# Kernel optimization log

Measured on AMD Instinct MI355X. Metric: run time of the kernel, lower is better.

The kernel has to match this reference:

```python
import jax, jax.numpy as jnp
import numpy as np

N_Q = 4; K = 4; IMG = 28; PAD = IMG + 2  # pad right/bottom so edge windows exist
N_WIN = 14 * 14  # stride-2 windows over 28x28


def _window_idx():
    # Faithful to torch: flatten the (possibly truncated) window row-major,
    # then pad with zeros AT THE END of the flattened vector.
    zero = PAD * PAD - 1  # padded image is zero there
    rows = []
    for i in range(0, IMG - 1, 2):
        for j in range(0, IMG - 1, 2):
            h = min(K, IMG - i); w = min(K, IMG - j)
            ids = [(i + r) * PAD + (j + c) for r in range(h) for c in range(w)]
            ids += [zero] * (K * K - len(ids))
            rows.append(ids)
    return np.asarray(rows, np.int32)  # [196, 16]

_WIDX = _window_idx()
# wire 0 is the most-significant bit of the 16-dim statevector index
_BITS = ((np.arange(16)[None, :] >> (3 - np.arange(4))[:, None]) & 1)
_ZSIGN = (1.0 - 2.0 * _BITS).astype(np.float32)  # [4, 16] PauliZ eigenvalues
# Four CRZ gates (control i, target (i+1)%4) are all diagonal -> combined diagonal phase
_CRZ_SIGNS = np.zeros(16, np.float32)
for _b in range(16):
    s = 0
    for _i in range(4):
        c = (_b >> (3 - _i)) & 1
        t = (_b >> (3 - ((_i + 1) % 4))) & 1
        s += c * (2 * t - 1)
    _CRZ_SIGNS[_b] = s
_H = (np.array([[1, 1], [1, -1]], np.complex64) / np.sqrt(2.0)).astype(np.complex64)


def _rz(a):  # a [B] -> [B,2,2]: diag(e^{-i a/2}, e^{+i a/2})
    em = jnp.exp(-0.5j * a); ep = jnp.exp(0.5j * a); z = jnp.zeros_like(em)
    return jnp.stack([jnp.stack([em, z], -1), jnp.stack([z, ep], -1)], -2)


def _ry(a):  # a [...] -> [...,2,2]
    c = jnp.cos(0.5 * a); s = jnp.sin(0.5 * a)
    return jnp.stack([jnp.stack([c, -s], -1), jnp.stack([s, c], -1)], -2).astype(jnp.complex64)


def _apply1q(state, U, w):  # state [B,16], U [B,2,2] or [2,2], wire w (0=MSB)
    L = 2 ** w; R = 2 ** (3 - w)
    s = state.reshape(-1, L, 2, R)
    if U.ndim == 2:
        out = jnp.einsum('ij,bajc->baic', U, s)
    else:
        out = jnp.einsum('bij,bajc->baic', U, s)
    return out.reshape(-1, 16)


def reference(x, crz_theta, ry_theta, fc1_w, fc1_b, fc2_w, fc2_b):
    B = x.shape[0]
    xp = jnp.pad(x[:, 0], ((0, 0), (0, 2), (0, 2))).reshape(B, -1)  # [B, 900]
    wins = xp[:, jnp.asarray(_WIDX)]              # [B, 196, 16]
    wins = jnp.transpose(wins, (1, 0, 2))         # [196, B, 16] for scan

    crz_diag = jnp.exp(0.5j * crz_theta * jnp.asarray(_CRZ_SIGNS))  # [16]
    Ry = _ry(ry_theta)                            # shared trainable RY, [2,2]
    H = jnp.asarray(_H)
    zsT = jnp.asarray(_ZSIGN).T                   # [16, 4]

    def step(state, f):  # state [B,16] complex64 persists ACROSS windows (no reset in source)
        for w in range(4):
            # compose H then the encoder rotations on this wire into one 2x2 per batch elem
            U = jnp.broadcast_to(H, (B, 2, 2))
            n = 5 if w < 3 else 1  # wire 3 only gets rz(f[15])
            for i in range(n):
                a = f[:, w * 5 + i]
                M = _rz(a) if i % 2 == 0 else _ry(a)  # gates = rz,ry,rz,ry,rz
                U = jnp.einsum('bij,bjk->bik', M, U)
            state = _apply1q(state, U, w)
        state = state * crz_diag[None, :]          # ring of CRZ gates (diagonal)
        for w in range(4):
            state = _apply1q(state, Ry, w)
        probs = state.real ** 2 + state.imag ** 2
        return state, probs @ zsT                  # [B, 4] PauliZ expectations

    state0 = jnp.zeros((B, 16), jnp.complex64).at[:, 0].set(1.0)
    _, outs = jax.lax.scan(step, state0, wins)     # [196, B, 4]
    feats = jnp.transpose(outs, (1, 0, 2)).reshape(B, N_WIN * 4)  # window-major concat
    h1 = feats @ fc1_w.T + fc1_b
    h1 = jnp.where(h1 > 0, h1, 0.1 * h1)           # LeakyReLU(0.1)
    return h1 @ fc2_w.T + fc2_b


def setup_inputs() -> dict:
    key = jax.random.key(0)
    ks = jax.random.split(key, 7)
    B = 16384
    return {
        'x': jax.random.normal(ks[0], (B, 1, 28, 28), jnp.float32),
        'crz_theta': jax.random.normal(ks[1], (), jnp.float32),
        'ry_theta': jax.random.normal(ks[2], (), jnp.float32),
        'fc1_w': jax.random.normal(ks[3], (20, 784), jnp.float32) * 0.03,
        'fc1_b': jnp.zeros((20,), jnp.float32),
        'fc2_w': jax.random.normal(ks[4], (2, 20), jnp.float32) * 0.1,
        'fc2_b': jnp.zeros((2,), jnp.float32),
    }
```

## Files before the change

### kernel.cpp

```cpp
#include <hip/hip_runtime.h>

#define RS2f 0.70710678118654752f

#define QP_XOR1 0xB1
#define QP_XOR2 0x4E
#define QP_BC0  0x00
#define QP_BC1  0x55
#define QP_BC2  0xAA
#define QP_BC3  0xFF

typedef float v2f __attribute__((ext_vector_type(2)));

template<int CTRL> __device__ __forceinline__ float dppf(float x) {
  return __int_as_float(__builtin_amdgcn_update_dpp(
      0, __float_as_int(x), CTRL, 0xF, 0xF, true));
}
template<int CTRL> __device__ __forceinline__ v2f dpp2(v2f v) {
  v2f r; r.x = dppf<CTRL>(v.x); r.y = dppf<CTRL>(v.y); return r;
}

__device__ __forceinline__ float sxor(float x, int sm) {
  return __int_as_float(__float_as_int(x) ^ sm);
}
__device__ __forceinline__ v2f vsplat(float a) { v2f r; r.x = a; r.y = a; return r; }
__device__ __forceinline__ v2f vperp(v2f v) { v2f r; r.x = -v.y; r.y = v.x; return r; }
__device__ __forceinline__ v2f vperc(v2f v) { v2f r; r.x = v.y; r.y = -v.x; return r; }
__device__ __forceinline__ v2f vfma2(float a, v2f b, v2f c) {
  return __builtin_elementwise_fma(vsplat(a), b, c);
}
__device__ __forceinline__ v2f vmul2(float a, v2f b) { return vsplat(a) * b; }

__device__ __forceinline__ void build_gate(float a0, float a1, float a2, float a3, float a4,
                                           float &w0r, float &w0i, float &w1r, float &w1i) {
  float sBp, cBp, sBm, cBm, sC, cC, sP, cP, sM, cM;
  __sincosf(0.5f * (a1 + a3), &sBp, &cBp);
  __sincosf(0.5f * (a1 - a3), &sBm, &cBm);
  __sincosf(0.5f * a2,        &sC,  &cC);
  __sincosf(0.5f * (a0 + a4), &sP,  &cP);
  __sincosf(0.5f * (a0 - a4), &sM,  &cM);
  float m00r =  cBp * cC, m00i = -cBm * sC;
  float m01r = -sBp * cC, m01i =  sBm * sC;
  float alr = fmaf(m00r, cP,  m00i * sP);
  float ali = fmaf(m00i, cP, -m00r * sP);
  float ber = fmaf(m01r, cM, -m01i * sM);
  float bei = fmaf(m01i, cM,  m01r * sM);
  w0r = RS2f * (alr + ber); w0i = RS2f * (ali + bei);
  w1r = RS2f * (alr - ber); w1i = RS2f * (ali - bei);
}

#define PICK_FULL                                                            \
  a0 = l0 ? P[0][0] : l1 ? P[1][1] : l2 ? P[2][2] : P[3][3];                 \
  a1 = l0 ? P[0][1] : l1 ? P[1][2] : l2 ? P[2][3] : 0.f;                     \
  a2 = l0 ? P[0][2] : l1 ? P[1][3] : l2 ? P[3][0] : 0.f;                     \
  a3 = l0 ? P[0][3] : l1 ? P[2][0] : l2 ? P[3][1] : 0.f;                     \
  a4 = l0 ? P[1][0] : l1 ? P[2][1] : l2 ? P[3][2] : 0.f;

#define PICK_W2                                                              \
  a0 = l0 ? P[0][0] : l1 ? P[2][1] : 0.f;                                    \
  a1 = l0 ? P[0][1] : l1 ? P[3][0] : 0.f;                                    \
  a2 = l0 ? P[1][0] : l1 ? P[3][1] : 0.f;                                    \
  a3 = l0 ? P[1][1] : 0.f;                                                   \
  a4 = l0 ? P[2][0] : 0.f;

#define PICK_H2                                                              \
  a0 = l0 ? P[0][0] : l1 ? P[1][1] : 0.f;                                    \
  a1 = l0 ? P[0][1] : l1 ? P[1][2] : 0.f;                                    \
  a2 = l0 ? P[0][2] : l1 ? P[1][3] : 0.f;                                    \
  a3 = l0 ? P[0][3] : 0.f;                                                   \
  a4 = l0 ? P[1][0] : 0.f;

#define PICK_22                                                              \
  a0 = l0 ? P[0][0] : 0.f;                                                   \
  a1 = l0 ? P[0][1] : 0.f;                                                   \
  a2 = l0 ? P[1][0] : 0.f;                                                   \
  a3 = l0 ? P[1][1] : 0.f;                                                   \
  a4 = 0.f;

#define APPLY_AND_FOLD(WIN) do {                                             \
                                \
  { float w0r = dppf<QP_BC0>(Wc0), w0i = dppf<QP_BC0>(Wc1);                  \
    float w1r = dppf<QP_BC0>(Wc2), w1i = dppf<QP_BC0>(Wc3);                  \
    float uar = sxor(w0r, sm0), uai = w0i;                                   \
    float ubr = w1r,            ubi = sxor(w1i, sm0);                        \
    _Pragma("unroll")                                                        \
    for (int k = 0; k < 4; ++k) {                                            \
      v2f p = dpp2<QP_XOR2>(s[k]);                                           \
      v2f a = s[k];                                                          \
      s[k] = vfma2(uar, a, vfma2(uai, vperp(a),                              \
                   vfma2(ubr, p, vmul2(ubi, vperp(p)))));                    \
    } }                                                                      \
                                 \
  { float w0r = dppf<QP_BC1>(Wc0), w0i = dppf<QP_BC1>(Wc1);                  \
    float w1r = dppf<QP_BC1>(Wc2), w1i = dppf<QP_BC1>(Wc3);                  \
    float uar = sxor(w0r, sm1), uai = w0i;                                   \
    float ubr = w1r,            ubi = sxor(w1i, sm1);                        \
    _Pragma("unroll")                                                        \
    for (int k = 0; k < 4; ++k) {                                            \
      v2f p = dpp2<QP_XOR1>(s[k]);                                           \
      v2f a = s[k];                                                          \
      s[k] = vfma2(uar, a, vfma2(uai, vperp(a),                              \
                   vfma2(ubr, p, vmul2(ubi, vperp(p)))));                    \
    } }                                                                      \
   \
  { float w0r = dppf<QP_BC2>(Wc0), w0i = dppf<QP_BC2>(Wc1);                  \
    float w1r = dppf<QP_BC2>(Wc2), w1i = dppf<QP_BC2>(Wc3);                  \
    float nw0r = -w0r, nw0i = -w0i;                                          \
    _Pragma("unroll")                                                        \
    for (int k = 0; k < 2; ++k) {                                            \
      v2f lo = s[k], hi = s[k+2];                                            \
      s[k]   = vfma2(w0r, lo, vfma2(w0i, vperp(lo),                          \
                     vfma2(w1r, hi, vmul2(w1i, vperp(hi)))));                \
      s[k+2] = vfma2(w1r, lo, vfma2(w1i, vperc(lo),                          \
                     vfma2(nw0r, hi, vmul2(nw0i, vperc(hi)))));              \
    } }                                                                      \
                                           \
  { float w0r = dppf<QP_BC3>(Wc0), w0i = dppf<QP_BC3>(Wc1);                  \
    float w1r = dppf<QP_BC3>(Wc2), w1i = dppf<QP_BC3>(Wc3);                  \
    float nw0r = -w0r, nw0i = -w0i;                                          \
    _Pragma("unroll")                                                        \
    for (int k = 0; k < 4; k += 2) {                                         \
      v2f lo = s[k], hi = s[k+1];                                            \
      s[k]   = vfma2(w0r, lo, vfma2(w0i, vperp(lo),                          \
                     vfma2(w1r, hi, vmul2(w1i, vperp(hi)))));                \
      s[k+1] = vfma2(w1r, lo, vfma2(w1i, vperc(lo),                          \
                     vfma2(nw0r, hi, vmul2(nw0i, vperc(hi)))));              \
    } }                                                                      \
                                    \
  _Pragma("unroll")                                                          \
  for (int k = 0; k < 4; ++k)                                                \
    s[k] = vfma2(czk[k], s[k], vmul2(szk[k], vperp(s[k])));                  \
                                              \
  _Pragma("unroll")                                                          \
  for (int k = 0; k < 4; ++k) {                                              \
    v2f p = dpp2<QP_XOR2>(s[k]);                                             \
    s[k] = vfma2(cry, s[k], vmul2(sgn0, p));                                 \
  }                                                                          \
  _Pragma("unroll")                                                          \
  for (int k = 0; k < 4; ++k) {                                              \
    v2f p = dpp2<QP_XOR1>(s[k]);                                             \
    s[k] = vfma2(cry, s[k], vmul2(sgn1, p));                                 \
  }                                                                          \
                                                   \
  _Pragma("unroll")                                                          \
  for (int k = 0; k < 2; ++k) {                                              \
    v2f lo = s[k], hi = s[k+2];                                              \
    s[k]   = vfma2(cry, lo, vmul2(nsry, hi));                                \
    s[k+2] = vfma2(sry, lo, vmul2(cry, hi));                                 \
  }                                                                          \
  _Pragma("unroll")                                                          \
  for (int k = 0; k < 4; k += 2) {                                           \
    v2f lo = s[k], hi = s[k+1];                                              \
    s[k]   = vfma2(cry, lo, vmul2(nsry, hi));                                \
    s[k+1] = vfma2(sry, lo, vmul2(cry, hi));                                 \
  }                                                                          \
                                        \
  { v2f q0 = s[0]*s[0], q1 = s[1]*s[1], q2 = s[2]*s[2], q3 = s[3]*s[3];      \
    float p0 = q0.x + q0.y, p1 = q1.x + q1.y;                                \
    float p2 = q2.x + q2.y, p3 = q3.x + q3.y;                                \
    float s01 = p0 + p1, s23 = p2 + p3;                                      \
    float t_  = s01 + s23;                                                   \
    float o0 = sxor(t_, sm0);                                                \
    float o1 = sxor(t_, sm1);                                                \
    float o2 = s01 - s23;                                                    \
    float o3 = (p0 - p1) + (p2 - p3);                                        \
    o0 += dppf<QP_XOR1>(o0); o0 += dppf<QP_XOR2>(o0);                        \
    o1 += dppf<QP_XOR1>(o1); o1 += dppf<QP_XOR2>(o1);                        \
    o2 += dppf<QP_XOR1>(o2); o2 += dppf<QP_XOR2>(o2);                        \
    o3 += dppf<QP_XOR1>(o3); o3 += dppf<QP_XOR2>(o3);                        \
    const int win4_ = (WIN) * 4;                                             \
    _Pragma("unroll")                                                        \
    for (int j = 0; j < 5; ++j) {                                            \
      float4 wv = *(const float4*)(swl + j * 784 + win4_);                   \
      h1[j] = fmaf(wv.x, o0, fmaf(wv.y, o1, fmaf(wv.z, o2, fmaf(wv.w, o3, h1[j])))); \
    } }                                                                      \
} while (0)

#define ROTATE_W  Wc0 = Wn0; Wc1 = Wn1; Wc2 = Wn2; Wc3 = Wn3;

__global__ void __launch_bounds__(256)
quanv_kernel(const float* __restrict__ x,
             const float* __restrict__ crz_t,
             const float* __restrict__ ry_t,
             const float* __restrict__ fc1_w,
             const float* __restrict__ fc1_b,
             const float* __restrict__ fc2_w,
             const float* __restrict__ fc2_b,
             float* __restrict__ out, int B)
{
  __shared__ float sw[20 * 784];
  const int tid = threadIdx.x;
  for (int i = tid; i < (20 * 784) / 4; i += 256)
    ((float4*)sw)[i] = ((const float4*)fc1_w)[i];
  __syncthreads();

  const int l = tid & 3;
  const int b = (blockIdx.x * 256 + tid) >> 2;
  if (b >= B) return;
  const float* img = x + (size_t)b * 784;
  const bool l0 = (l == 0), l1 = (l == 1), l2 = (l == 2);

  const float theta = crz_t[0];
  const float ryt   = ry_t[0];
  float cry, sry;
  __sincosf(0.5f * ryt, &sry, &cry);
  const float nsry = -sry;
  const float sgn0 = (l & 2) ? sry : -sry;
  const float sgn1 = (l & 1) ? sry : -sry;
  const int sm0 = (l & 2) ? (int)0x80000000 : 0;
  const int sm1 = (l & 1) ? (int)0x80000000 : 0;

  float g0,g1,g2,g3;
  if      (l == 0) { g0= 0.f; g1=-1.f; g2=-1.f; g3=0.f; }
  else if (l == 1) { g0=-1.f; g1=-2.f; g2= 0.f; g3=1.f; }
  else if (l == 2) { g0=-1.f; g1= 0.f; g2=-2.f; g3=1.f; }
  else             { g0= 0.f; g1= 1.f; g2= 1.f; g3=4.f; }
  float czk[4], szk[4];
  __sincosf(0.5f*theta*g0, &szk[0], &czk[0]);
  __sincosf(0.5f*theta*g1, &szk[1], &czk[1]);
  __sincosf(0.5f*theta*g2, &szk[2], &czk[2]);
  __sincosf(0.5f*theta*g3, &szk[3], &czk[3]);

  v2f s[4];
#pragma unroll
  for (int k = 0; k < 4; ++k) { s[k].x = 0.f; s[k].y = 0.f; }
  if (l == 0) s[0].x = 1.f;

  float h1[5];
#pragma unroll
  for (int j = 0; j < 5; ++j) h1[j] = 0.f;
  const float* swl = sw + 5 * l * 784;

  float P[4][4];
  float a0, a1, a2, a3, a4;
  float Wc0, Wc1, Wc2, Wc3, Wn0, Wn1, Wn2, Wn3;

#pragma unroll 1
  for (int wi = 0; wi < 13; ++wi) {
    const float* imgw = img + (2 * wi) * 28;

#pragma unroll
    for (int r = 0; r < 4; ++r) {
      float4 v = *(const float4*)(imgw + r * 28);
      P[r][0]=v.x; P[r][1]=v.y; P[r][2]=v.z; P[r][3]=v.w;
    }
    PICK_FULL;
    build_gate(a0, a1, a2, a3, a4, Wc0, Wc1, Wc2, Wc3);

#pragma unroll 1
    for (int wj = 1; wj <= 12; ++wj) {
      const int c0 = 2 * wj + 2;
#pragma unroll
      for (int r = 0; r < 4; ++r) {
        P[r][0] = P[r][2]; P[r][1] = P[r][3];
        float2 v = *(const float2*)(imgw + r * 28 + c0);
        P[r][2] = v.x; P[r][3] = v.y;
      }
      PICK_FULL;
      build_gate(a0, a1, a2, a3, a4, Wn0, Wn1, Wn2, Wn3);
      APPLY_AND_FOLD(wi * 14 + wj - 1);
      ROTATE_W;
    }

#pragma unroll
    for (int r = 0; r < 4; ++r) {
      P[r][0] = P[r][2]; P[r][1] = P[r][3]; P[r][2] = 0.f; P[r][3] = 0.f;
    }
    PICK_W2;
    build_gate(a0, a1, a2, a3, a4, Wn0, Wn1, Wn2, Wn3);
    APPLY_AND_FOLD(wi * 14 + 12);
    ROTATE_W;
    APPLY_AND_FOLD(wi * 14 + 13);
  }

  {
    const float* imgw = img + 26 * 28;
#pragma unroll
    for (int r = 0; r < 2; ++r) {
      float4 v = *(const float4*)(imgw + r * 28);
      P[r][0]=v.x; P[r][1]=v.y; P[r][2]=v.z; P[r][3]=v.w;
    }
#pragma unroll
    for (int r = 2; r < 4; ++r) { P[r][0]=0.f; P[r][1]=0.f; P[r][2]=0.f; P[r][3]=0.f; }
    PICK_H2;
    build_gate(a0, a1, a2, a3, a4, Wc0, Wc1, Wc2, Wc3);

#pragma unroll 1
    for (int wj = 1; wj <= 12; ++wj) {
      const int c0 = 2 * wj + 2;
      P[0][0]=P[0][2]; P[0][1]=P[0][3];
      P[1][0]=P[1][2]; P[1][1]=P[1][3];
      float2 v0 = *(const float2*)(imgw + c0);       P[0][2]=v0.x; P[0][3]=v0.y;
      float2 v1 = *(const float2*)(imgw + 28 + c0);  P[1][2]=v1.x; P[1][3]=v1.y;
      PICK_H2;
      build_gate(a0, a1, a2, a3, a4, Wn0, Wn1, Wn2, Wn3);
      APPLY_AND_FOLD(182 + wj - 1);
      ROTATE_W;
    }

    P[0][0]=P[0][2]; P[0][1]=P[0][3]; P[0][2]=0.f; P[0][3]=0.f;
    P[1][0]=P[1][2]; P[1][1]=P[1][3]; P[1][2]=0.f; P[1][3]=0.f;
    PICK_22;
    build_gate(a0, a1, a2, a3, a4, Wn0, Wn1, Wn2, Wn3);
    APPLY_AND_FOLD(182 + 12);
    ROTATE_W;
    APPLY_AND_FOLD(182 + 13);
  }

  float pa = 0.f, pb = 0.f;
#pragma unroll
  for (int j = 0; j < 5; ++j) {
    const int r = 5 * l + j;
    float v = h1[j] + fc1_b[r];
    v = (v > 0.f) ? v : 0.1f * v;
    pa = fmaf(fc2_w[r],      v, pa);
    pb = fmaf(fc2_w[20 + r], v, pb);
  }
  pa += dppf<QP_XOR1>(pa); pa += dppf<QP_XOR2>(pa);
  pb += dppf<QP_XOR1>(pb); pb += dppf<QP_XOR2>(pb);
  if (l == 0) {
    float2 res; res.x = pa + fc2_b[0]; res.y = pb + fc2_b[1];
    *(float2*)(out + (size_t)b * 2) = res;
  }
}

extern "C" void kernel_launch(void* const* d_in, const int* in_sizes, int n_in,
                              void* d_out, int out_size, void* d_ws, size_t ws_size,
                              hipStream_t stream) {
  const float* x      = (const float*)d_in[0];
  const float* crz_t  = (const float*)d_in[1];
  const float* ry_t   = (const float*)d_in[2];
  const float* fc1_w  = (const float*)d_in[3];
  const float* fc1_b  = (const float*)d_in[4];
  const float* fc2_w  = (const float*)d_in[5];
  const float* fc2_b  = (const float*)d_in[6];
  float* out = (float*)d_out;
  const int B = in_sizes[0] / 784;
  const int grid = (B * 4 + 255) / 256;
  quanv_kernel<<<grid, 256, 0, stream>>>(x, crz_t, ry_t, fc1_w, fc1_b,
                                         fc2_w, fc2_b, out, B);
}
```

Measured before the change: 225.0 us.

## Split each statevector across eight lanes instead of four

Each sample now runs on 8 lanes holding 2 amplitudes each instead of 4 lanes holding 4, so the grid doubles. The third qubit's exchange uses ds_swizzle with XOR 4, and the fc1 rows are split so each lane accumulates 3 (or 2) hidden units. The aim is more parallelism and fewer registers per thread. In exchange, every lane now repeats the gate construction and image loads, and each step adds extra cross-lane swizzle work.

```diff
diff --git a/kernel.cpp b/kernel.cpp
--- a/kernel.cpp
+++ b/kernel.cpp
@@ -9,6 +9,8 @@
 #define QP_BC2  0xAA
 #define QP_BC3  0xFF
 
+#define SWZ_XOR4 0x101F
+
 typedef float v2f __attribute__((ext_vector_type(2)));
 
 template<int CTRL> __device__ __forceinline__ float dppf(float x) {
@@ -17,6 +19,12 @@
 }
 template<int CTRL> __device__ __forceinline__ v2f dpp2(v2f v) {
   v2f r; r.x = dppf<CTRL>(v.x); r.y = dppf<CTRL>(v.y); return r;
+}
+__device__ __forceinline__ float swzf4(float x) {
+  return __int_as_float(__builtin_amdgcn_ds_swizzle(__float_as_int(x), SWZ_XOR4));
+}
+__device__ __forceinline__ v2f swz4v(v2f v) {
+  v2f r; r.x = swzf4(v.x); r.y = swzf4(v.y); return r;
 }
 
 __device__ __forceinline__ float sxor(float x, int sm) {
@@ -77,102 +85,92 @@
   a4 = 0.f;
 
 #define APPLY_AND_FOLD(WIN) do {                                             \
-                                \
+                     \
   { float w0r = dppf<QP_BC0>(Wc0), w0i = dppf<QP_BC0>(Wc1);                  \
     float w1r = dppf<QP_BC0>(Wc2), w1i = dppf<QP_BC0>(Wc3);                  \
-    float uar = sxor(w0r, sm0), uai = w0i;                                   \
-    float ubr = w1r,            ubi = sxor(w1i, sm0);                        \
-    _Pragma("unroll")                                                        \
-    for (int k = 0; k < 4; ++k) {                                            \
-      v2f p = dpp2<QP_XOR2>(s[k]);                                           \
-      v2f a = s[k];                                                          \
-      s[k] = vfma2(uar, a, vfma2(uai, vperp(a),                              \
-                   vfma2(ubr, p, vmul2(ubi, vperp(p)))));                    \
-    } }                                                                      \
-                                 \
+    float uar = sxor(w0r, smA), uai = w0i;                                   \
+    float ubr = w1r,            ubi = sxor(w1i, smA);                        \
+    v2f p0 = swz4v(s[0]), p1 = swz4v(s[1]);                                  \
+    v2f a0_ = s[0], a1_ = s[1];                                              \
+    s[0] = vfma2(uar, a0_, vfma2(uai, vperp(a0_),                            \
+                 vfma2(ubr, p0, vmul2(ubi, vperp(p0)))));                    \
+    s[1] = vfma2(uar, a1_, vfma2(uai, vperp(a1_),                            \
+                 vfma2(ubr, p1, vmul2(ubi, vperp(p1)))));                    \
+  }                                                                          \
+                            \
   { float w0r = dppf<QP_BC1>(Wc0), w0i = dppf<QP_BC1>(Wc1);                  \
     float w1r = dppf<QP_BC1>(Wc2), w1i = dppf<QP_BC1>(Wc3);                  \
-    float uar = sxor(w0r, sm1), uai = w0i;                                   \
-    float ubr = w1r,            ubi = sxor(w1i, sm1);                        \
-    _Pragma("unroll")                                                        \
-    for (int k = 0; k < 4; ++k) {                                            \
-      v2f p = dpp2<QP_XOR1>(s[k]);                                           \
-      v2f a = s[k];                                                          \
-      s[k] = vfma2(uar, a, vfma2(uai, vperp(a),                              \
-                   vfma2(ubr, p, vmul2(ubi, vperp(p)))));                    \
-    } }                                                                      \
-   \
+    float uar = sxor(w0r, smB), uai = w0i;                                   \
+    float ubr = w1r,            ubi = sxor(w1i, smB);                        \
+    v2f p0 = dpp2<QP_XOR2>(s[0]), p1 = dpp2<QP_XOR2>(s[1]);                  \
+    v2f a0_ = s[0], a1_ = s[1];                                              \
+    s[0] = vfma2(uar, a0_, vfma2(uai, vperp(a0_),                            \
+                 vfma2(ubr, p0, vmul2(ubi, vperp(p0)))));                    \
+    s[1] = vfma2(uar, a1_, vfma2(uai, vperp(a1_),                            \
+                 vfma2(ubr, p1, vmul2(ubi, vperp(p1)))));                    \
+  }                                                                          \
+                            \
   { float w0r = dppf<QP_BC2>(Wc0), w0i = dppf<QP_BC2>(Wc1);                  \
     float w1r = dppf<QP_BC2>(Wc2), w1i = dppf<QP_BC2>(Wc3);                  \
-    float nw0r = -w0r, nw0i = -w0i;                                          \
-    _Pragma("unroll")                                                        \
-    for (int k = 0; k < 2; ++k) {                                            \
-      v2f lo = s[k], hi = s[k+2];                                            \
-      s[k]   = vfma2(w0r, lo, vfma2(w0i, vperp(lo),                          \
-                     vfma2(w1r, hi, vmul2(w1i, vperp(hi)))));                \
-      s[k+2] = vfma2(w1r, lo, vfma2(w1i, vperc(lo),                          \
-                     vfma2(nw0r, hi, vmul2(nw0i, vperc(hi)))));              \
-    } }                                                                      \
-                                           \
+    float uar = sxor(w0r, smC), uai = w0i;                                   \
+    float ubr = w1r,            ubi = sxor(w1i, smC);                        \
+    v2f p0 = dpp2<QP_XOR1>(s[0]), p1 = dpp2<QP_XOR1>(s[1]);                  \
+    v2f a0_ = s[0], a1_ = s[1];                                              \
+    s[0] = vfma2(uar, a0_, vfma2(uai, vperp(a0_),                            \
+                 vfma2(ubr, p0, vmul2(ubi, vperp(p0)))));                    \
+    s[1] = vfma2(uar, a1_, vfma2(uai, vperp(a1_),                            \
+                 vfma2(ubr, p1, vmul2(ubi, vperp(p1)))));                    \
+  }                                                                          \
+                            \
   { float w0r = dppf<QP_BC3>(Wc0), w0i = dppf<QP_BC3>(Wc1);                  \
     float w1r = dppf<QP_BC3>(Wc2), w1i = dppf<QP_BC3>(Wc3);                  \
     float nw0r = -w0r, nw0i = -w0i;                                          \
-    _Pragma("unroll")                                                        \
-    for (int k = 0; k < 4; k += 2) {                                         \
-      v2f lo = s[k], hi = s[k+1];                                            \
-      s[k]   = vfma2(w0r, lo, vfma2(w0i, vperp(lo),                          \
-                     vfma2(w1r, hi, vmul2(w1i, vperp(hi)))));                \
-      s[k+1] = vfma2(w1r, lo, vfma2(w1i, vperc(lo),                          \
-                     vfma2(nw0r, hi, vmul2(nw0i, vperc(hi)))));              \
-    } }                                                                      \
-                                    \
-  _Pragma("unroll")                                                          \
-  for (int k = 0; k < 4; ++k)                                                \
-    s[k] = vfma2(czk[k], s[k], vmul2(szk[k], vperp(s[k])));                  \
+    v2f lo = s[0], hi = s[1];                                                \
+    s[0] = vfma2(w0r, lo, vfma2(w0i, vperp(lo),                              \
+                 vfma2(w1r, hi, vmul2(w1i, vperp(hi)))));                    \
+    s[1] = vfma2(w1r, lo, vfma2(w1i, vperc(lo),                              \
+                 vfma2(nw0r, hi, vmul2(nw0i, vperc(hi)))));                  \
+  }                                                                          \
+                                                      \
+  s[0] = vfma2(cz0, s[0], vmul2(sz0, vperp(s[0])));                          \
+  s[1] = vfma2(cz1, s[1], vmul2(sz1, vperp(s[1])));                          \
                                               \
-  _Pragma("unroll")                                                          \
-  for (int k = 0; k < 4; ++k) {                                              \
-    v2f p = dpp2<QP_XOR2>(s[k]);                                             \
-    s[k] = vfma2(cry, s[k], vmul2(sgn0, p));                                 \
-  }                                                                          \
-  _Pragma("unroll")                                                          \
-  for (int k = 0; k < 4; ++k) {                                              \
-    v2f p = dpp2<QP_XOR1>(s[k]);                                             \
-    s[k] = vfma2(cry, s[k], vmul2(sgn1, p));                                 \
-  }                                                                          \
-                                                   \
-  _Pragma("unroll")                                                          \
-  for (int k = 0; k < 2; ++k) {                                              \
-    v2f lo = s[k], hi = s[k+2];                                              \
-    s[k]   = vfma2(cry, lo, vmul2(nsry, hi));                                \
-    s[k+2] = vfma2(sry, lo, vmul2(cry, hi));                                 \
-  }                                                                          \
-  _Pragma("unroll")                                                          \
-  for (int k = 0; k < 4; k += 2) {                                           \
-    v2f lo = s[k], hi = s[k+1];                                              \
-    s[k]   = vfma2(cry, lo, vmul2(nsry, hi));                                \
-    s[k+1] = vfma2(sry, lo, vmul2(cry, hi));                                 \
-  }                                                                          \
-                                        \
-  { v2f q0 = s[0]*s[0], q1 = s[1]*s[1], q2 = s[2]*s[2], q3 = s[3]*s[3];      \
+  { v2f p0 = swz4v(s[0]), p1 = swz4v(s[1]);                                  \
+    s[0] = vfma2(cry, s[0], vmul2(sgnA, p0));                                \
+    s[1] = vfma2(cry, s[1], vmul2(sgnA, p1)); }                              \
+                                                  \
+  { v2f p0 = dpp2<QP_XOR2>(s[0]), p1 = dpp2<QP_XOR2>(s[1]);                  \
+    s[0] = vfma2(cry, s[0], vmul2(sgnB, p0));                                \
+    s[1] = vfma2(cry, s[1], vmul2(sgnB, p1)); }                              \
+                                                  \
+  { v2f p0 = dpp2<QP_XOR1>(s[0]), p1 = dpp2<QP_XOR1>(s[1]);                  \
+    s[0] = vfma2(cry, s[0], vmul2(sgnC, p0));                                \
+    s[1] = vfma2(cry, s[1], vmul2(sgnC, p1)); }                              \
+                                                       \
+  { v2f lo = s[0], hi = s[1];                                                \
+    s[0] = vfma2(cry, lo, vmul2(nsry, hi));                                  \
+    s[1] = vfma2(sry, lo, vmul2(cry, hi)); }                                 \
+       \
+  { v2f q0 = s[0]*s[0], q1 = s[1]*s[1];                                      \
     float p0 = q0.x + q0.y, p1 = q1.x + q1.y;                                \
-    float p2 = q2.x + q2.y, p3 = q3.x + q3.y;                                \
-    float s01 = p0 + p1, s23 = p2 + p3;                                      \
-    float t_  = s01 + s23;                                                   \
-    float o0 = sxor(t_, sm0);                                                \
-    float o1 = sxor(t_, sm1);                                                \
-    float o2 = s01 - s23;                                                    \
-    float o3 = (p0 - p1) + (p2 - p3);                                        \
-    o0 += dppf<QP_XOR1>(o0); o0 += dppf<QP_XOR2>(o0);                        \
-    o1 += dppf<QP_XOR1>(o1); o1 += dppf<QP_XOR2>(o1);                        \
-    o2 += dppf<QP_XOR1>(o2); o2 += dppf<QP_XOR2>(o2);                        \
-    o3 += dppf<QP_XOR1>(o3); o3 += dppf<QP_XOR2>(o3);                        \
+    float t_ = p0 + p1;                                                      \
+    float o0 = sxor(t_, smA);                                                \
+    float o1 = sxor(t_, smB);                                                \
+    float o2 = sxor(t_, smC);                                                \
+    float o3 = p0 - p1;                                                      \
+    o0 += dppf<QP_XOR1>(o0); o1 += dppf<QP_XOR1>(o1);                        \
+    o2 += dppf<QP_XOR1>(o2); o3 += dppf<QP_XOR1>(o3);                        \
+    o0 += dppf<QP_XOR2>(o0); o1 += dppf<QP_XOR2>(o1);                        \
+    o2 += dppf<QP_XOR2>(o2); o3 += dppf<QP_XOR2>(o3);                        \
+    o0 += swzf4(o0); o1 += swzf4(o1); o2 += swzf4(o2); o3 += swzf4(o3);      \
     const int win4_ = (WIN) * 4;                                             \
-    _Pragma("unroll")                                                        \
-    for (int j = 0; j < 5; ++j) {                                            \
-      float4 wv = *(const float4*)(swl + j * 784 + win4_);                   \
-      h1[j] = fmaf(wv.x, o0, fmaf(wv.y, o1, fmaf(wv.z, o2, fmaf(wv.w, o3, h1[j])))); \
-    } }                                                                      \
+    float4 wv0 = *(const float4*)(swl + win4_);                              \
+    float4 wv1 = *(const float4*)(swl + 784 + win4_);                        \
+    float4 wv2 = *(const float4*)(swl + off2 + win4_);                       \
+    h1[0] = fmaf(wv0.x, o0, fmaf(wv0.y, o1, fmaf(wv0.z, o2, fmaf(wv0.w, o3, h1[0])))); \
+    h1[1] = fmaf(wv1.x, o0, fmaf(wv1.y, o1, fmaf(wv1.z, o2, fmaf(wv1.w, o3, h1[1])))); \
+    h1[2] = fmaf(wv2.x, o0, fmaf(wv2.y, o1, fmaf(wv2.z, o2, fmaf(wv2.w, o3, h1[2])))); \
+  }                                                                          \
 } while (0)
 
 #define ROTATE_W  Wc0 = Wn0; Wc1 = Wn1; Wc2 = Wn2; Wc3 = Wn3;
@@ -193,42 +191,42 @@
     ((float4*)sw)[i] = ((const float4*)fc1_w)[i];
   __syncthreads();
 
-  const int l = tid & 3;
-  const int b = (blockIdx.x * 256 + tid) >> 2;
+  const int L = tid & 7;
+  const int b = (blockIdx.x * 256 + tid) >> 3;
   if (b >= B) return;
   const float* img = x + (size_t)b * 784;
-  const bool l0 = (l == 0), l1 = (l == 1), l2 = (l == 2);
+  const int w_ = L & 3;
+  const bool l0 = (w_ == 0), l1 = (w_ == 1), l2 = (w_ == 2);
+  const int hiH = L >> 2;
 
   const float theta = crz_t[0];
   const float ryt   = ry_t[0];
   float cry, sry;
   __sincosf(0.5f * ryt, &sry, &cry);
   const float nsry = -sry;
-  const float sgn0 = (l & 2) ? sry : -sry;
-  const float sgn1 = (l & 1) ? sry : -sry;
-  const int sm0 = (l & 2) ? (int)0x80000000 : 0;
-  const int sm1 = (l & 1) ? (int)0x80000000 : 0;
-
-  float g0,g1,g2,g3;
-  if      (l == 0) { g0= 0.f; g1=-1.f; g2=-1.f; g3=0.f; }
-  else if (l == 1) { g0=-1.f; g1=-2.f; g2= 0.f; g3=1.f; }
-  else if (l == 2) { g0=-1.f; g1= 0.f; g2=-2.f; g3=1.f; }
-  else             { g0= 0.f; g1= 1.f; g2= 1.f; g3=4.f; }
-  float czk[4], szk[4];
-  __sincosf(0.5f*theta*g0, &szk[0], &czk[0]);
-  __sincosf(0.5f*theta*g1, &szk[1], &czk[1]);
-  __sincosf(0.5f*theta*g2, &szk[2], &czk[2]);
-  __sincosf(0.5f*theta*g3, &szk[3], &czk[3]);
-
-  v2f s[4];
-#pragma unroll
-  for (int k = 0; k < 4; ++k) { s[k].x = 0.f; s[k].y = 0.f; }
-  if (l == 0) s[0].x = 1.f;
-
-  float h1[5];
-#pragma unroll
-  for (int j = 0; j < 5; ++j) h1[j] = 0.f;
-  const float* swl = sw + 5 * l * 784;
+  const float sgnA = (L & 4) ? sry : -sry;
+  const float sgnB = (L & 2) ? sry : -sry;
+  const float sgnC = (L & 1) ? sry : -sry;
+  const int smA = (L & 4) ? (int)0x80000000 : 0;
+  const int smB = (L & 2) ? (int)0x80000000 : 0;
+  const int smC = (L & 1) ? (int)0x80000000 : 0;
+
+  const float gk0 = (L==1||L==2||L==4) ? -1.f : (L==5) ? -2.f : (L==7) ? 1.f : 0.f;
+  const float gk1 = (L==0) ? -1.f : (L==2) ? -2.f :
+                    (L==3||L==5||L==6) ? 1.f : (L==7) ? 4.f : 0.f;
+  float cz0, sz0, cz1, sz1;
+  __sincosf(0.5f*theta*gk0, &sz0, &cz0);
+  __sincosf(0.5f*theta*gk1, &sz1, &cz1);
+
+  v2f s[2];
+  s[0].x = 0.f; s[0].y = 0.f; s[1].x = 0.f; s[1].y = 0.f;
+  if (L == 0) s[0].x = 1.f;
+
+  const int row0 = 5 * w_ + (hiH ? 3 : 0);
+  const int off2 = hiH ? 784 : 1568;
+  float h1[3];
+  h1[0] = 0.f; h1[1] = 0.f; h1[2] = 0.f;
+  const float* swl = sw + row0 * 784;
 
   float P[4][4];
   float a0, a1, a2, a3, a4;
@@ -307,17 +305,27 @@
   }
 
   float pa = 0.f, pb = 0.f;
-#pragma unroll
-  for (int j = 0; j < 5; ++j) {
-    const int r = 5 * l + j;
-    float v = h1[j] + fc1_b[r];
+  {
+    int r = row0;
+    float v = h1[0] + fc1_b[r];
     v = (v > 0.f) ? v : 0.1f * v;
-    pa = fmaf(fc2_w[r],      v, pa);
-    pb = fmaf(fc2_w[20 + r], v, pb);
-  }
-  pa += dppf<QP_XOR1>(pa); pa += dppf<QP_XOR2>(pa);
-  pb += dppf<QP_XOR1>(pb); pb += dppf<QP_XOR2>(pb);
-  if (l == 0) {
+    pa = fmaf(fc2_w[r], v, pa); pb = fmaf(fc2_w[20 + r], v, pb);
+  }
+  {
+    int r = row0 + 1;
+    float v = h1[1] + fc1_b[r];
+    v = (v > 0.f) ? v : 0.1f * v;
+    pa = fmaf(fc2_w[r], v, pa); pb = fmaf(fc2_w[20 + r], v, pb);
+  }
+  if (!hiH) {
+    int r = row0 + 2;
+    float v = h1[2] + fc1_b[r];
+    v = (v > 0.f) ? v : 0.1f * v;
+    pa = fmaf(fc2_w[r], v, pa); pb = fmaf(fc2_w[20 + r], v, pb);
+  }
+  pa += dppf<QP_XOR1>(pa); pa += dppf<QP_XOR2>(pa); pa += swzf4(pa);
+  pb += dppf<QP_XOR1>(pb); pb += dppf<QP_XOR2>(pb); pb += swzf4(pb);
+  if (L == 0) {
     float2 res; res.x = pa + fc2_b[0]; res.y = pb + fc2_b[1];
     *(float2*)(out + (size_t)b * 2) = res;
   }
@@ -335,7 +343,7 @@
   const float* fc2_b  = (const float*)d_in[6];
   float* out = (float*)d_out;
   const int B = in_sizes[0] / 784;
-  const int grid = (B * 4 + 255) / 256;
+  const int grid = (B * 8 + 255) / 256;
   quanv_kernel<<<grid, 256, 0, stream>>>(x, crz_t, ry_t, fc1_w, fc1_b,
                                          fc2_w, fc2_b, out, B);
 }
```

After: 263.7 us. 17.2% more time.
